# Optimization experiments

Hardware: AMD Instinct MI355X
Metric: run time of the kernel (lower is better)

## Reference

```python
import jax, jax.numpy as jnp
import numpy as np

B, S, D, H = 2, 2048, 1024, 16
HEAD_DIM = D // H
THETA = 10000.0


def setup_inputs() -> dict:
    key = jax.random.key(0)
    kx, kq, kk, kv, ko = jax.random.split(key, 5)
    w_scale = jnp.float32(D ** -0.5)  # keep logits O(1)
    return {
        "x": jax.random.normal(kx, (B, S, D), dtype=jnp.float32),
        "WQ": jax.random.normal(kq, (D, D), dtype=jnp.float32) * w_scale,
        "WK": jax.random.normal(kk, (D, D), dtype=jnp.float32) * w_scale,
        "WV": jax.random.normal(kv, (D, D), dtype=jnp.float32) * w_scale,
        "WO": jax.random.normal(ko, (D, D), dtype=jnp.float32) * w_scale,
        "token_positions": jnp.arange(S, dtype=jnp.int32),
    }


def _rope(x, pos, theta):
    # x: [B, H, S, dh]; pos: [S]. Interleaved (even, odd) pair rotation.
    dh = x.shape[-1]
    inv_freq = theta ** (-jnp.arange(0, dh, 2, dtype=jnp.float32) / dh)  # [dh/2]
    ang = pos.astype(jnp.float32)[:, None] * inv_freq                    # [S, dh/2]
    cos, sin = jnp.cos(ang), jnp.sin(ang)
    x1, x2 = x[..., 0::2], x[..., 1::2]
    r1 = x1 * cos - x2 * sin
    r2 = x1 * sin + x2 * cos
    return jnp.stack([r1, r2], axis=-1).reshape(x.shape)


def reference(x, WQ, WK, WV, WO, token_positions):
    Bs, Ss, Dm = x.shape
    dh = Dm // H
    # QKV projections (Linear with no bias, y = x @ W.T), split heads -> [B,H,S,dh]
    q = (x @ WQ.T).reshape(Bs, Ss, H, dh).transpose(0, 2, 1, 3)
    k = (x @ WK.T).reshape(Bs, Ss, H, dh).transpose(0, 2, 1, 3)
    v = (x @ WV.T).reshape(Bs, Ss, H, dh).transpose(0, 2, 1, 3)
    q = _rope(q, token_positions, THETA)
    k = _rope(k, token_positions, THETA)
    scores = jnp.einsum("bhqd,bhkd->bhqk", q, k) * jnp.float32(dh ** -0.5)
    causal = jnp.tril(jnp.ones((Ss, Ss), dtype=bool))
    scores = jnp.where(causal, scores, jnp.finfo(scores.dtype).min)
    attn = jax.nn.softmax(scores, axis=-1)
    out = jnp.einsum("bhqk,bhkd->bhqd", attn, v)
    out = out.transpose(0, 2, 1, 3).reshape(Bs, Ss, Dm)
    return out @ WO.T
```

## Files before the change

### kernel.cpp

```cpp
#include <hip/hip_runtime.h>
#include <hip/hip_bf16.h>


#define S_LEN 2048
#define NEG_SENT -30000.0f

typedef __attribute__((ext_vector_type(8))) short short8;
typedef __attribute__((ext_vector_type(4))) float f32x4;
typedef unsigned int u32;
typedef unsigned short u16;

static __device__ __forceinline__ float bf2f(u16 u) {
  union { u32 i; float f; } v; v.i = ((u32)u) << 16; return v.f;
}
static __device__ __forceinline__ u16 f2bf(float f) {
  union { float f; u32 i; } v; v.f = f;
  u32 u = v.i;
  u32 r = (u + 0x7fffu + ((u >> 16) & 1u)) >> 16;
  return (u16)r;
}
static __device__ __forceinline__ u32 cvtpk(float a, float b) {
  u32 r;
  asm("v_cvt_pk_bf16_f32 %0, %1, %2" : "=v"(r) : "v"(a), "v"(b));
  return r;
}

static __device__ __forceinline__ void glds16(const void* g, void* l) {
  __builtin_amdgcn_global_load_lds((const __attribute__((address_space(1))) u32*)g,
                                   (__attribute__((address_space(3))) u32*)l, 16, 0, 0);
}

__global__ void convert_kernel(const float* __restrict__ x, const float* __restrict__ wq,
                               const float* __restrict__ wk, const float* __restrict__ wv,
                               const float* __restrict__ wo, const int* __restrict__ pos,
                               u16* __restrict__ xb, u16* __restrict__ wb,
                               float2* __restrict__ tab) {
  const int stride = gridDim.x * blockDim.x;
  for (int i = blockIdx.x * blockDim.x + threadIdx.x; i < 2162688; i += stride) {
    if (i >= 2097152) {
      int e = i - 2097152;
      int s = e >> 5, ip = e & 31;
      float p = (float)pos[s];
      float ang = p * __builtin_exp2f((float)ip * -0.41524101186f);
      float sn, cs;
      sincosf(ang, &sn, &cs);
      tab[e] = make_float2(cs, sn);
      continue;
    }
    const float* src; u16* dst; int off;
    if (i < 1048576) { src = x; dst = xb; off = i; }
    else {
      int j = i - 1048576;
      int widx = j >> 18;
      off = j & 262143;
      src = (widx == 0) ? wq : (widx == 1) ? wk : (widx == 2) ? wv : wo;
      dst = wb + (size_t)widx * 1048576;
    }
    float4 v = ((const float4*)src)[off];
    ushort4 o;
    o.x = f2bf(v.x); o.y = f2bf(v.y); o.z = f2bf(v.z); o.w = f2bf(v.w);
    ((ushort4*)dst)[off] = o;
  }
}

__global__ __launch_bounds__(256, 2) void gemm_qkv(const u16* __restrict__ A,
                                                   const u16* __restrict__ B,
                                                   u16* __restrict__ o0, u16* __restrict__ o1,
                                                   u16* __restrict__ o2,
                                                   const float2* __restrict__ tab, int K) {
  __shared__ __align__(16) u16 AsBs[2 * 128 * 64];
  u16* const As = AsBs;
  u16* const Bs = AsBs + 128 * 64;
  const int tid = threadIdx.x, w = tid >> 6, l = tid & 63, l15 = l & 15, l4 = l >> 4;
  const int wr = w >> 1, wc = w & 1;
  const int lid = blockIdx.y * gridDim.x + blockIdx.x;
  const int xcd = lid & 7;
  const int jj2 = lid >> 3;
  const int mrows = gridDim.y >> 3;
  const int m0 = (xcd * mrows + jj2 / gridDim.x) << 7;
  const int n0 = (jj2 % gridDim.x) << 7;
  const int r = tid >> 3;
  const int swcol = ((tid & 7) << 4) ^ ((r & 7) << 4);
  const char* Ag = (const char*)A + (((size_t)(m0 + r) * K) << 1) + swcol;
  const char* Bg = (const char*)B + (((size_t)(n0 + r) * K) << 1) + swcol;
  char* AsW = (char*)As + (w << 10);
  char* BsW = (char*)Bs + (w << 10);
  const size_t rowskip = ((size_t)32 * K) << 1;
  f32x4 acc[4][4] = {};
  for (int k0 = 0; k0 < K; k0 += 64) {
    __syncthreads();
    const size_t kb = (size_t)k0 << 1;
#pragma unroll
    for (int i = 0; i < 4; i++) {
      glds16(Ag + kb + (size_t)i * rowskip, AsW + i * 4096);
      glds16(Bg + kb + (size_t)i * rowskip, BsW + i * 4096);
    }
    __syncthreads();
#pragma unroll
    for (int kk = 0; kk < 2; kk++) {
      short8 a[4], b[4];
#pragma unroll
      for (int m = 0; m < 4; m++) {
        int row = (wr << 6) + (m << 4) + l15;
        a[m] = *(const short8*)((const char*)As + row * 128 +
                                (((kk << 6) + (l4 << 4)) ^ ((row & 7) << 4)));
      }
#pragma unroll
      for (int n = 0; n < 4; n++) {
        int row = (wc << 6) + (n << 4) + l15;
        b[n] = *(const short8*)((const char*)Bs + row * 128 +
                                (((kk << 6) + (l4 << 4)) ^ ((row & 7) << 4)));
      }
#pragma unroll
      for (int m = 0; m < 4; m++)
#pragma unroll
        for (int n = 0; n < 4; n++)
          acc[m][n] = __builtin_amdgcn_mfma_f32_16x16x32_bf16(a[m], b[n], acc[m][n], 0, 0, 0);
    }
  }
  if (n0 >= 2048) {
    __syncthreads();
    u16* T = AsBs;
#pragma unroll
    for (int m = 0; m < 4; m++)
#pragma unroll
      for (int n = 0; n < 4; n++) {
        int ct = (wc << 6) + (n << 4) + l15;
#pragma unroll
        for (int j = 0; j < 4; j++) {
          int rt = (wr << 6) + (m << 4) + (l4 << 2) + j;
          T[rt * 128 + (ct ^ (((rt >> 6) & 1) << 1))] = f2bf(acc[m][n][j]);
        }
      }
    __syncthreads();
    const int d = tid >> 1, sh = tid & 1;
    const int dr = d ^ (sh << 1);
    const int bb = m0 >> 11;
    const int colv = (n0 & 1023) + d;
    const int row = (((bb << 4) | (colv >> 6)) << 6) | (colv & 63);
    u16* dst = o2 + ((size_t)row << 11) + (m0 & (S_LEN - 1)) + (sh << 6);
#pragma unroll
    for (int k8 = 0; k8 < 8; k8++) {
      u16 tmp[8];
#pragma unroll
      for (int e = 0; e < 8; e++) tmp[e] = T[((sh << 6) + (k8 << 3) + e) * 128 + dr];
      *(uint4*)(dst + (k8 << 3)) = *(const uint4*)tmp;
    }
    return;
  }
#pragma unroll
  for (int m = 0; m < 4; m++) {
    int grow_b = m0 + (wr << 6) + (m << 4) + (l4 << 2);
#pragma unroll
    for (int n = 0; n < 4; n++) {
      int gcol = n0 + (wc << 6) + (n << 4) + l15;
      const float qscale = (gcol < 1024) ? 0.125f * 1.44269504089f : 1.f;
      u16* base = (gcol < 1024) ? o0 : o1;
      const int col = gcol & 1023;
      const int d = col & 63;
      const float sgn = (d & 1) ? 1.f : -1.f;
      const int ip = d >> 1;
#pragma unroll
      for (int j = 0; j < 4; j++) {
        int grow = grow_b + j;
        float v = acc[m][n][j] * qscale;
        float pv = __shfl_xor(v, 1, 64);
        float2 cssn = tab[((grow & (S_LEN - 1)) << 5) + ip];
        base[((size_t)grow << 10) + col] = f2bf(v * cssn.x + pv * cssn.y * sgn);
      }
    }
  }
}

__global__ __launch_bounds__(256, 2) void gemm_wo(const u16* __restrict__ A,
                                                  const u16* __restrict__ B,
                                                  float* __restrict__ oF, int K) {
  __shared__ __align__(16) u16 AsBs[(64 + 128) * 64];
  u16* const As = AsBs;
  u16* const Bs = AsBs + 64 * 64;
  const int tid = threadIdx.x, w = tid >> 6, l = tid & 63, l15 = l & 15, l4 = l >> 4;
  const int wr = w >> 1, wc = w & 1;
  const int lid = blockIdx.y * gridDim.x + blockIdx.x;
  const int xcd = lid & 7;
  const int jj2 = lid >> 3;
  const int mrows = gridDim.y >> 3;
  const int m0 = (xcd * mrows + jj2 / gridDim.x) << 6;
  const int n0 = (jj2 % gridDim.x) << 7;
  const int r = tid >> 3;
  const int swcol = ((tid & 7) << 4) ^ ((r & 7) << 4);
  const char* Ag = (const char*)A + (((size_t)(m0 + r) * K) << 1) + swcol;
  const char* Bg = (const char*)B + (((size_t)(n0 + r) * K) << 1) + swcol;
  char* AsW = (char*)As + (w << 10);
  char* BsW = (char*)Bs + (w << 10);
  const size_t rowskip = ((size_t)32 * K) << 1;
  f32x4 acc[2][4] = {};
  for (int k0 = 0; k0 < K; k0 += 64) {
    __syncthreads();
    const size_t kb = (size_t)k0 << 1;
    glds16(Ag + kb, AsW);
    glds16(Ag + kb + rowskip, AsW + 4096);
#pragma unroll
    for (int i = 0; i < 4; i++)
      glds16(Bg + kb + (size_t)i * rowskip, BsW + i * 4096);
    __syncthreads();
#pragma unroll
    for (int kk = 0; kk < 2; kk++) {
      short8 a[2], b[4];
#pragma unroll
      for (int m = 0; m < 2; m++) {
        int row = (wr << 5) + (m << 4) + l15;
        a[m] = *(const short8*)((const char*)As + row * 128 +
                                (((kk << 6) + (l4 << 4)) ^ ((row & 7) << 4)));
      }
#pragma unroll
      for (int n = 0; n < 4; n++) {
        int row = (wc << 6) + (n << 4) + l15;
        b[n] = *(const short8*)((const char*)Bs + row * 128 +
                                (((kk << 6) + (l4 << 4)) ^ ((row & 7) << 4)));
      }
#pragma unroll
      for (int m = 0; m < 2; m++)
#pragma unroll
        for (int n = 0; n < 4; n++)
          acc[m][n] = __builtin_amdgcn_mfma_f32_16x16x32_bf16(a[m], b[n], acc[m][n], 0, 0, 0);
    }
  }
#pragma unroll
  for (int m = 0; m < 2; m++) {
    int grow_b = m0 + (wr << 5) + (m << 4) + (l4 << 2);
#pragma unroll
    for (int n = 0; n < 4; n++) {
      int gcol = n0 + (wc << 6) + (n << 4) + l15;
#pragma unroll
      for (int j = 0; j < 4; j++)
        oF[((size_t)(grow_b + j) << 10) + gcol] = acc[m][n][j];
    }
  }
}

__global__ __launch_bounds__(512, 1) void attn_kernel(const u16* __restrict__ Q,
                                                      const u16* __restrict__ K,
                                                      const u16* __restrict__ Vt,
                                                      u16* __restrict__ O) {
  extern __shared__ __align__(16) char smem[];
  const int tid = threadIdx.x, w = tid >> 6, l = tid & 63, l15 = l & 15, g = l >> 4;
  const int grp = w >> 2, w4 = w & 3;
  const int i = blockIdx.x;
  const int xcd = i & 7, slot = i >> 3;
  const int bh = ((slot >> 3) << 3) | xcd;
  const int p = slot & 7;
  const int b = bh >> 4, h = bh & 15;
  const int swz = (l15 & 7) << 4;

  const int gt = tid & 255;
  const int r = gt >> 3;
  const int kr = ((r & 28) << 1) | (r & 3);
  const int swc = ((gt & 7) << 4) ^ ((r & 7) << 4);
  const char* Kg = (const char*)K + ((size_t)(b * S_LEN + kr) << 11) + (h << 7) + swc;
  const char* Vg = (const char*)Vt + ((size_t)((bh << 6) + r) << 12) + swc;
  char* const KsG = smem + (grp << 16);
  char* const VsG = smem + (grp << 16) + 32768;
  float* const oMrg = (float*)smem;
  float* const lMrg = (float*)(smem + 131072);

#define STAGE2(PI, BSEL)                                            \
  do {                                                              \
    char* kd = KsG + ((BSEL) << 14) + (w4 << 10);                   \
    char* vd = VsG + ((BSEL) << 14) + (w4 << 10);                   \
    const char* ks = Kg + ((size_t)(PI) << 18);                     \
    const char* vs = Vg + ((PI) << 8);                              \
    glds16(ks, kd);                                                 \
    glds16(ks + (4 << 11), kd + 4096);                              \
    glds16(ks + (64 << 11), kd + 8192);                             \
    glds16(ks + (68 << 11), kd + 12288);                            \
    glds16(vs, vd);                                                 \
    glds16(vs + ((size_t)32 << 12), vd + 4096);                     \
    glds16(vs + 128, vd + 8192);                                    \
    glds16(vs + 128 + ((size_t)32 << 12), vd + 12288);              \
  } while (0)

  auto run_qt = [&](int qt) {
    const int q0 = qt << 7;
    const int nr = (qt + 2) >> 1;

    short8 aQ[2][2];
    {
      const int qrow0 = q0 + (w4 << 5) + l15;
      const u16* qp = Q + (((size_t)(b * S_LEN + qrow0)) << 10) + (h << 6) + (g << 3);
      aQ[0][0] = *(const short8*)qp;
      aQ[0][1] = *(const short8*)(qp + 32);
      aQ[1][0] = *(const short8*)(qp + (16 << 10));
      aQ[1][1] = *(const short8*)(qp + (16 << 10) + 32);
    }
    f32x4 o[2][4] = {};
    float l_r[2] = {0.f, 0.f};

    auto subtile = [&](int t, const char* Kbuf, const char* Vbuf, bool domask) {
      f32x4 s[2][4] = {};
#pragma unroll
      for (int kk = 0; kk < 2; ++kk) {
        short8 aK[4];
#pragma unroll
        for (int n = 0; n < 4; ++n) {
          int row = (n << 4) + l15;
          aK[n] = *(const short8*)(Kbuf + row * 128 + (((kk << 6) + (g << 4)) ^ swz));
        }
        __builtin_amdgcn_s_setprio(1);
#pragma unroll
        for (int n = 0; n < 4; ++n) {
          s[0][n] = __builtin_amdgcn_mfma_f32_16x16x32_bf16(aK[n], aQ[0][kk], s[0][n], 0, 0, 0);
          s[1][n] = __builtin_amdgcn_mfma_f32_16x16x32_bf16(aK[n], aQ[1][kk], s[1][n], 0, 0, 0);
        }
        __builtin_amdgcn_s_setprio(0);
      }
      if (domask) {
#pragma unroll
        for (int qs = 0; qs < 2; ++qs) {
          int qg = q0 + (w4 << 5) + (qs << 4) + l15;
#pragma unroll
          for (int n = 0; n < 4; ++n)
#pragma unroll
            for (int jj = 0; jj < 4; ++jj) {
              int key = (t << 6) + ((n & 1) << 5) + (g << 3) + ((n >> 1) << 2) + jj;
              if (key > qg) s[qs][n][jj] = NEG_SENT;
            }
        }
      }
      short8 aP[2][2];
#pragma unroll
      for (int qs = 0; qs < 2; ++qs) {
        float p_[4][4];
        float rs = 0.f;
#pragma unroll
        for (int n = 0; n < 4; ++n) {
#pragma unroll
          for (int jj = 0; jj < 4; ++jj) {
            p_[n][jj] = __builtin_exp2f(s[qs][n][jj]);
            rs += p_[n][jj];
          }
        }
        l_r[qs] += rs;
#pragma unroll
        for (int kk = 0; kk < 2; ++kk) {
          union { u32 u[4]; short8 v; } wd;
#pragma unroll
          for (int wi = 0; wi < 4; ++wi) {
            const int nw = ((wi >> 1) << 1) | kk;
            wd.u[wi] = cvtpk(p_[nw][(wi & 1) * 2], p_[nw][(wi & 1) * 2 + 1]);
          }
          aP[qs][kk] = wd.v;
        }
      }
#pragma unroll
      for (int kk = 0; kk < 2; ++kk) {
        int co = (kk << 6) + (g << 4);
        __builtin_amdgcn_s_setprio(1);
#pragma unroll
        for (int nd = 0; nd < 4; ++nd) {
          int row = (nd << 4) + l15;
          short8 bV = *(const short8*)(Vbuf + row * 128 + (co ^ swz));
          o[0][nd] = __builtin_amdgcn_mfma_f32_16x16x32_bf16(aP[0][kk], bV, o[0][nd], 0, 0, 0);
          o[1][nd] = __builtin_amdgcn_mfma_f32_16x16x32_bf16(aP[1][kk], bV, o[1][nd], 0, 0, 0);
        }
        __builtin_amdgcn_s_setprio(0);
      }
    };

    if (grp <= qt) STAGE2(grp, 0);
    __syncthreads();

    for (int rr = 0; rr < nr; ++rr) {
      const int bsel = rr & 1;
      const int pi = 2 * rr + grp;
      if (pi + 2 <= qt) STAGE2(pi + 2, bsel ^ 1);
      if (pi <= qt) {
        const char* Kb0 = KsG + (bsel << 14);
        const char* Vb0 = VsG + (bsel << 14);
        const bool dm = (pi == qt);
        const bool lowW = (w4 < 2);
        subtile(2 * pi, Kb0, Vb0, dm && lowW);
        if (!(dm && lowW))
          subtile(2 * pi + 1, Kb0 + 8192, Vb0 + 8192, dm);
      }
      __syncthreads();
    }

    if (grp == 1) {
      float* ob = oMrg + (w4 << 11);
#pragma unroll
      for (int qs = 0; qs < 2; ++qs)
#pragma unroll
        for (int nd = 0; nd < 4; ++nd)
          *(f32x4*)(ob + (((qs << 2) | nd) << 8) + (l << 2)) = o[qs][nd];
      float* lb = lMrg + (w4 << 7);
      lb[l] = l_r[0];
      lb[64 + l] = l_r[1];
    }
    __syncthreads();
    if (grp == 0) {
      float* ob = oMrg + (w4 << 11);
      float* lb = lMrg + (w4 << 7);
#pragma unroll
      for (int qs = 0; qs < 2; ++qs) {
        float lsum = l_r[qs] + lb[(qs << 6) + l];
        lsum += __shfl_xor(lsum, 16);
        lsum += __shfl_xor(lsum, 32);
        float linv = 1.f / lsum;
        f32x4 oB[4];
#pragma unroll
        for (int nd = 0; nd < 4; ++nd)
          oB[nd] = *(const f32x4*)(ob + (((qs << 2) | nd) << 8) + (l << 2));
#pragma unroll
        for (int jj = 0; jj < 4; ++jj) {
          float lo = __shfl(linv, (g << 2) + jj, 16);
          int qg = q0 + (w4 << 5) + (qs << 4) + (g << 2) + jj;
          u16* orow = O + (((size_t)(b * S_LEN + qg)) << 10) + (h << 6) + l15;
#pragma unroll
          for (int nd = 0; nd < 4; ++nd)
            orow[nd << 4] = f2bf((o[qs][nd][jj] + oB[nd][jj]) * lo);
        }
      }
    }
    __syncthreads();
  };

  run_qt(p);
  run_qt(15 - p);
#undef STAGE2
}

extern "C" void kernel_launch(void* const* d_in, const int* in_sizes, int n_in,
                              void* d_out, int out_size, void* d_ws, size_t ws_size,
                              hipStream_t stream) {
  (void)in_sizes; (void)n_in; (void)out_size; (void)ws_size;
  const float* x = (const float*)d_in[0];
  const float* wq = (const float*)d_in[1];
  const float* wk = (const float*)d_in[2];
  const float* wv = (const float*)d_in[3];
  const float* wo = (const float*)d_in[4];
  const int* pos = (const int*)d_in[5];
  char* ws = (char*)d_ws;
  u16* xb = (u16*)ws;
  u16* wb = (u16*)(ws + ((size_t)8 << 20));
  u16* Qb = (u16*)(ws + ((size_t)16 << 20));
  u16* Kb = (u16*)(ws + ((size_t)24 << 20));
  u16* Vtg = (u16*)(ws + ((size_t)32 << 20));
  u16* Ab = (u16*)(ws + ((size_t)40 << 20));
  float* out = (float*)d_out;
  float2* tab = (float2*)d_out;

  convert_kernel<<<2112, 256, 0, stream>>>(x, wq, wk, wv, wo, pos, xb, wb, tab);
  dim3 g1(24, 32);
  gemm_qkv<<<g1, 256, 0, stream>>>(xb, wb, Qb, Kb, Vtg, tab, 1024);
  attn_kernel<<<256, 512, 135168, stream>>>(Qb, Kb, Vtg, Ab);
  dim3 g3(8, 64);
  gemm_wo<<<g3, 256, 0, stream>>>(Ab, wb + (size_t)3 * 1048576, out, 1024);
}
```

Measured before the change: 97.53 us.

## Halve attention K/V staging to one 64-key subtile per group per round

Each of the two wave groups now stages and processes a single 64-key subtile per loop iteration instead of a 128-key pair. This halves the shared-memory footprint (about 66 KB instead of 132 KB), and launch bounds are raised to allow more resident blocks per CU. The intent is higher occupancy and better latency hiding. The cost is twice as many loop iterations and barriers per query tile. The register cap implied by the new launch bound may also cause spills.

```diff
diff --git a/kernel.cpp b/kernel.cpp
--- a/kernel.cpp
+++ b/kernel.cpp
@@ -238,7 +238,7 @@
   }
 }
 
-__global__ __launch_bounds__(512, 1) void attn_kernel(const u16* __restrict__ Q,
+__global__ __launch_bounds__(512, 4) void attn_kernel(const u16* __restrict__ Q,
                                                       const u16* __restrict__ K,
                                                       const u16* __restrict__ Vt,
                                                       u16* __restrict__ O) {
@@ -258,30 +258,27 @@
   const int swc = ((gt & 7) << 4) ^ ((r & 7) << 4);
   const char* Kg = (const char*)K + ((size_t)(b * S_LEN + kr) << 11) + (h << 7) + swc;
   const char* Vg = (const char*)Vt + ((size_t)((bh << 6) + r) << 12) + swc;
-  char* const KsG = smem + (grp << 16);
-  char* const VsG = smem + (grp << 16) + 32768;
+  char* const KsG = smem + (grp << 15);
+  char* const VsG = smem + (grp << 15) + 16384;
   float* const oMrg = (float*)smem;
-  float* const lMrg = (float*)(smem + 131072);
-
-#define STAGE2(PI, BSEL)                                            \
+  float* const lMrg = (float*)(smem + 65536);
+
+#define STAGE(T, BSEL)                                              \
   do {                                                              \
-    char* kd = KsG + ((BSEL) << 14) + (w4 << 10);                   \
-    char* vd = VsG + ((BSEL) << 14) + (w4 << 10);                   \
-    const char* ks = Kg + ((size_t)(PI) << 18);                     \
-    const char* vs = Vg + ((PI) << 8);                              \
+    char* kd = KsG + ((BSEL) << 13) + (w4 << 10);                   \
+    char* vd = VsG + ((BSEL) << 13) + (w4 << 10);                   \
+    const char* ks = Kg + ((size_t)(T) << 17);                      \
+    const char* vs = Vg + ((T) << 7);                               \
     glds16(ks, kd);                                                 \
     glds16(ks + (4 << 11), kd + 4096);                              \
-    glds16(ks + (64 << 11), kd + 8192);                             \
-    glds16(ks + (68 << 11), kd + 12288);                            \
     glds16(vs, vd);                                                 \
     glds16(vs + ((size_t)32 << 12), vd + 4096);                     \
-    glds16(vs + 128, vd + 8192);                                    \
-    glds16(vs + 128 + ((size_t)32 << 12), vd + 12288);              \
   } while (0)
 
   auto run_qt = [&](int qt) {
     const int q0 = qt << 7;
-    const int nr = (qt + 2) >> 1;
+    const int nt = (qt + 1) << 1;
+    const int nr = qt + 1;
 
     short8 aQ[2][2];
     {
@@ -366,21 +363,23 @@
       }
     };
 
-    if (grp <= qt) STAGE2(grp, 0);
+    if (grp < nt) STAGE(grp, 0);
     __syncthreads();
 
     for (int rr = 0; rr < nr; ++rr) {
       const int bsel = rr & 1;
-      const int pi = 2 * rr + grp;
-      if (pi + 2 <= qt) STAGE2(pi + 2, bsel ^ 1);
-      if (pi <= qt) {
-        const char* Kb0 = KsG + (bsel << 14);
-        const char* Vb0 = VsG + (bsel << 14);
-        const bool dm = (pi == qt);
+      const int t = 2 * rr + grp;
+      if (t + 2 < nt) STAGE(t + 2, bsel ^ 1);
+      {
+        const char* Kbuf = KsG + (bsel << 13);
+        const char* Vbuf = VsG + (bsel << 13);
+        const bool dm = (t >= nt - 2);
         const bool lowW = (w4 < 2);
-        subtile(2 * pi, Kb0, Vb0, dm && lowW);
-        if (!(dm && lowW))
-          subtile(2 * pi + 1, Kb0 + 8192, Vb0 + 8192, dm);
+        if (grp == 0) {
+          subtile(t, Kbuf, Vbuf, dm && lowW);
+        } else {
+          if (!(dm && lowW)) subtile(t, Kbuf, Vbuf, dm);
+        }
       }
       __syncthreads();
     }
@@ -426,7 +425,7 @@
 
   run_qt(p);
   run_qt(15 - p);
-#undef STAGE2
+#undef STAGE
 }
 
 extern "C" void kernel_launch(void* const* d_in, const int* in_sizes, int n_in,
@@ -452,7 +451,7 @@
   convert_kernel<<<2112, 256, 0, stream>>>(x, wq, wk, wv, wo, pos, xb, wb, tab);
   dim3 g1(24, 32);
   gemm_qkv<<<g1, 256, 0, stream>>>(xb, wb, Qb, Kb, Vtg, tab, 1024);
-  attn_kernel<<<256, 512, 135168, stream>>>(Qb, Kb, Vtg, Ab);
+  attn_kernel<<<256, 512, 67584, stream>>>(Qb, Kb, Vtg, Ab);
   dim3 g3(8, 64);
   gemm_wo<<<g3, 256, 0, stream>>>(Ab, wb + (size_t)3 * 1048576, out, 1024);
 }
```

New measurement: 108.1 us. 10.9% more time.
